# Kernel tuning notes

Measured on AMD Instinct MI355X. Metric: run time of the kernel, lower is better.

Reference implementation:

```python
import jax, jax.numpy as jnp
import numpy as np

KX = jnp.array([[-1., 0., 1.], [-2., 0., 2.], [-1., 0., 1.]], dtype=jnp.float32).reshape(1, 1, 3, 3)
KY = jnp.array([[1., 2., 1.], [0., 0., 0.], [-1., -2., -1.]], dtype=jnp.float32).reshape(1, 1, 3, 3)

def _sobel(x, k):
    # x: [B,1,H,W], k: [1,1,3,3]; stride 1, padding 1 -> same spatial size
    return jax.lax.conv_general_dilated(
        x, k, window_strides=(1, 1), padding=((1, 1), (1, 1)),
        dimension_numbers=('NCHW', 'OIHW', 'NCHW'))

def setup_inputs() -> dict:
    key = jax.random.key(0)
    k1, k2 = jax.random.split(key)
    B, C, H, W = 32, 1, 512, 512
    output = jax.random.normal(k1, (B, C, H, W), dtype=jnp.float32)
    target = jax.random.normal(k2, (B, C, H, W), dtype=jnp.float32)
    return {"output": output, "target": target}

def reference(output, target):
    gx_t = _sobel(target, KX)
    gy_t = _sobel(target, KY)
    gx_o = _sobel(output, KX)
    gy_o = _sobel(output, KY)
    grad_loss = jnp.mean((gx_t - gx_o) ** 2) + jnp.mean((gy_t - gy_o) ** 2)
    return grad_loss
```

## Files before the change

### kernel.cpp

```cpp
#include <hip/hip_runtime.h>


#define BATCH 32
#define HH 512
#define WW 512
#define RW 4
#define TPB 256
#define NBLK 1024
#define SPI (HH / RW)

__global__ __launch_bounds__(TPB) void sobel_partial_kernel(
    const float* __restrict__ out_img,
    const float* __restrict__ tgt_img,
    float* __restrict__ partials)
{
    const int tid  = threadIdx.x;
    const int lane = tid & 63;
    const int wv   = tid >> 6;
    const int b    = (blockIdx.x & 7) * (NBLK / 8) + (blockIdx.x >> 3);
    const int w    = b * (TPB / 64) + wv;
    const int img  = w >> 7;
    const int y0   = (w & (SPI - 1)) * RW;
    const size_t base = (size_t)img * HH * WW;
    const float* ob = out_img + base + (lane << 3);
    const float* tb = tgt_img + base + (lane << 3);

    float acc = 0.f;

#define DECLROW(j) float4 oA##j, oB##j, tA##j, tB##j, dA##j, dB##j,            \
                          hsA##j, hdA##j, hsB##j, hdB##j;

#define LOADR(j) {                                                             \
    const int gc = min(max(y0 - 1 + (j), 0), HH - 1);                          \
    const float* orow_ = ob + (size_t)gc * WW;                                 \
    const float* trow_ = tb + (size_t)gc * WW;                                 \
    oA##j = *(const float4*)orow_;       oB##j = *(const float4*)(orow_ + 4);  \
    tA##j = *(const float4*)trow_;       tB##j = *(const float4*)(trow_ + 4);  }

#define DIFFH(j) {                                                             \
    const float m_ = ((unsigned)(y0 - 1 + (j)) < (unsigned)HH) ? 1.f : 0.f;    \
    dA##j = make_float4(m_*(tA##j.x-oA##j.x), m_*(tA##j.y-oA##j.y),            \
                        m_*(tA##j.z-oA##j.z), m_*(tA##j.w-oA##j.w));           \
    dB##j = make_float4(m_*(tB##j.x-oB##j.x), m_*(tB##j.y-oB##j.y),            \
                        m_*(tB##j.z-oB##j.z), m_*(tB##j.w-oB##j.w));           \
    float dl_ = __shfl_up(dB##j.w, 1, 64);   if (lane == 0)  dl_ = 0.f;        \
    float dr_ = __shfl_down(dA##j.x, 1, 64); if (lane == 63) dr_ = 0.f;        \
    hsA##j.x = fmaf(2.f, dA##j.x, dl_ + dA##j.y);                              \
    hdA##j.x = dA##j.y - dl_;                                                  \
    hsA##j.y = fmaf(2.f, dA##j.y, dA##j.x + dA##j.z);                          \
    hdA##j.y = dA##j.z - dA##j.x;                                              \
    hsA##j.z = fmaf(2.f, dA##j.z, dA##j.y + dA##j.w);                          \
    hdA##j.z = dA##j.w - dA##j.y;                                              \
    hsA##j.w = fmaf(2.f, dA##j.w, dA##j.z + dB##j.x);                          \
    hdA##j.w = dB##j.x - dA##j.z;                                              \
    hsB##j.x = fmaf(2.f, dB##j.x, dA##j.w + dB##j.y);                          \
    hdB##j.x = dB##j.y - dA##j.w;                                              \
    hsB##j.y = fmaf(2.f, dB##j.y, dB##j.x + dB##j.z);                          \
    hdB##j.y = dB##j.z - dB##j.x;                                              \
    hsB##j.z = fmaf(2.f, dB##j.z, dB##j.y + dB##j.w);                          \
    hdB##j.z = dB##j.w - dB##j.y;                                              \
    hsB##j.w = fmaf(2.f, dB##j.w, dB##j.z + dr_);                              \
    hdB##j.w = dr_ - dB##j.z;                                                  }

#define VP1(S, a, bb, c) {                                                     \
    float gx_, gy_;                                                            \
    gx_ = fmaf(2.f, hd##S##bb.x, hd##S##a.x + hd##S##c.x);                     \
    gy_ = hs##S##a.x - hs##S##c.x;                                             \
    acc = fmaf(gx_, gx_, acc); acc = fmaf(gy_, gy_, acc);                      \
    gx_ = fmaf(2.f, hd##S##bb.y, hd##S##a.y + hd##S##c.y);                     \
    gy_ = hs##S##a.y - hs##S##c.y;                                             \
    acc = fmaf(gx_, gx_, acc); acc = fmaf(gy_, gy_, acc);                      \
    gx_ = fmaf(2.f, hd##S##bb.z, hd##S##a.z + hd##S##c.z);                     \
    gy_ = hs##S##a.z - hs##S##c.z;                                             \
    acc = fmaf(gx_, gx_, acc); acc = fmaf(gy_, gy_, acc);                      \
    gx_ = fmaf(2.f, hd##S##bb.w, hd##S##a.w + hd##S##c.w);                     \
    gy_ = hs##S##a.w - hs##S##c.w;                                             \
    acc = fmaf(gx_, gx_, acc); acc = fmaf(gy_, gy_, acc);                      }
#define VPASS(a, bb, c) VP1(A, a, bb, c) VP1(B, a, bb, c)

    DECLROW(0) DECLROW(1) DECLROW(2) DECLROW(3) DECLROW(4) DECLROW(5)

    LOADR(0) LOADR(1) LOADR(2) LOADR(3)
    DIFFH(0) DIFFH(1)
    LOADR(4)
    DIFFH(2) VPASS(0, 1, 2)
    LOADR(5)
    DIFFH(3) VPASS(1, 2, 3)
    DIFFH(4) VPASS(2, 3, 4)
    DIFFH(5) VPASS(3, 4, 5)

#undef DECLROW
#undef LOADR
#undef DIFFH
#undef VP1
#undef VPASS

    #pragma unroll
    for (int off = 32; off > 0; off >>= 1)
        acc += __shfl_down(acc, off, 64);
    __shared__ float wsum[TPB / 64];
    if (lane == 0) wsum[wv] = acc;
    __syncthreads();
    if (tid == 0)
        partials[b] = wsum[0] + wsum[1] + wsum[2] + wsum[3];
}

__global__ __launch_bounds__(TPB) void reduce_partials_kernel(
    const float* __restrict__ partials, float* __restrict__ out)
{
    const int tid = threadIdx.x;
    const float4 v = *(const float4*)(partials + tid * 4);
    float s = (v.x + v.y) + (v.z + v.w);
    #pragma unroll
    for (int off = 32; off > 0; off >>= 1)
        s += __shfl_down(s, off, 64);
    __shared__ float wsum[TPB / 64];
    if ((tid & 63) == 0) wsum[tid >> 6] = s;
    __syncthreads();
    if (tid == 0)
        out[0] = (wsum[0] + wsum[1] + wsum[2] + wsum[3])
               * (1.0f / ((float)BATCH * HH * WW));
}

extern "C" void kernel_launch(void* const* d_in, const int* in_sizes, int n_in,
                              void* d_out, int out_size, void* d_ws, size_t ws_size,
                              hipStream_t stream) {
    (void)in_sizes; (void)n_in; (void)ws_size; (void)out_size;
    const float* out_img = (const float*)d_in[0];
    const float* tgt_img = (const float*)d_in[1];
    float* partials = (float*)d_ws;
    float* res = (float*)d_out;

    sobel_partial_kernel<<<NBLK, TPB, 0, stream>>>(out_img, tgt_img, partials);
    reduce_partials_kernel<<<1, TPB, 0, stream>>>(partials, res);
}
```

Baseline: 18.62 us.

## Process eight rows per wave with rotating register ring and bigger blocks

Result: no change. 18.82 us (median of 2 runs) (+1.1%).

```diff
diff --git a/kernel.cpp b/kernel.cpp
--- a/kernel.cpp
+++ b/kernel.cpp
@@ -4,10 +4,9 @@
 #define BATCH 32
 #define HH 512
 #define WW 512
-#define RW 4
-#define TPB 256
-#define NBLK 1024
-#define SPI (HH / RW)
+#define RW 8
+#define TPB 512
+#define NBLK 256
 
 __global__ __launch_bounds__(TPB) void sobel_partial_kernel(
     const float* __restrict__ out_img,
@@ -18,81 +17,75 @@
     const int lane = tid & 63;
     const int wv   = tid >> 6;
     const int b    = (blockIdx.x & 7) * (NBLK / 8) + (blockIdx.x >> 3);
-    const int w    = b * (TPB / 64) + wv;
-    const int img  = w >> 7;
-    const int y0   = (w & (SPI - 1)) * RW;
+    const int img  = b >> 3;
+    const int y0   = ((b & 7) * 8 + wv) * RW;
     const size_t base = (size_t)img * HH * WW;
     const float* ob = out_img + base + (lane << 3);
     const float* tb = tgt_img + base + (lane << 3);
 
     float acc = 0.f;
 
-#define DECLROW(j) float4 oA##j, oB##j, tA##j, tB##j, dA##j, dB##j,            \
-                          hsA##j, hdA##j, hsB##j, hdB##j;
+#define DECLL(k) float4 oA##k, oB##k, tA##k, tB##k;
+#define DECLH(h) float4 hsA##h, hdA##h, hsB##h, hdB##h;
+    DECLL(0) DECLL(1) DECLL(2) DECLL(3)
+    DECLH(0) DECLH(1) DECLH(2)
 
-#define LOADR(j) {                                                             \
-    const int gc = min(max(y0 - 1 + (j), 0), HH - 1);                          \
-    const float* orow_ = ob + (size_t)gc * WW;                                 \
-    const float* trow_ = tb + (size_t)gc * WW;                                 \
-    oA##j = *(const float4*)orow_;       oB##j = *(const float4*)(orow_ + 4);  \
-    tA##j = *(const float4*)trow_;       tB##j = *(const float4*)(trow_ + 4);  }
+#define LOADR(i, k) {                                                          \
+    const int gc_ = min(max(y0 - 1 + (i), 0), HH - 1);                         \
+    const float* o_ = ob + (size_t)gc_ * WW;                                   \
+    const float* t_ = tb + (size_t)gc_ * WW;                                   \
+    oA##k = *(const float4*)o_;  oB##k = *(const float4*)(o_ + 4);             \
+    tA##k = *(const float4*)t_;  tB##k = *(const float4*)(t_ + 4);             }
 
-#define DIFFH(j) {                                                             \
-    const float m_ = ((unsigned)(y0 - 1 + (j)) < (unsigned)HH) ? 1.f : 0.f;    \
-    dA##j = make_float4(m_*(tA##j.x-oA##j.x), m_*(tA##j.y-oA##j.y),            \
-                        m_*(tA##j.z-oA##j.z), m_*(tA##j.w-oA##j.w));           \
-    dB##j = make_float4(m_*(tB##j.x-oB##j.x), m_*(tB##j.y-oB##j.y),            \
-                        m_*(tB##j.z-oB##j.z), m_*(tB##j.w-oB##j.w));           \
-    float dl_ = __shfl_up(dB##j.w, 1, 64);   if (lane == 0)  dl_ = 0.f;        \
-    float dr_ = __shfl_down(dA##j.x, 1, 64); if (lane == 63) dr_ = 0.f;        \
-    hsA##j.x = fmaf(2.f, dA##j.x, dl_ + dA##j.y);                              \
-    hdA##j.x = dA##j.y - dl_;                                                  \
-    hsA##j.y = fmaf(2.f, dA##j.y, dA##j.x + dA##j.z);                          \
-    hdA##j.y = dA##j.z - dA##j.x;                                              \
-    hsA##j.z = fmaf(2.f, dA##j.z, dA##j.y + dA##j.w);                          \
-    hdA##j.z = dA##j.w - dA##j.y;                                              \
-    hsA##j.w = fmaf(2.f, dA##j.w, dA##j.z + dB##j.x);                          \
-    hdA##j.w = dB##j.x - dA##j.z;                                              \
-    hsB##j.x = fmaf(2.f, dB##j.x, dA##j.w + dB##j.y);                          \
-    hdB##j.x = dB##j.y - dA##j.w;                                              \
-    hsB##j.y = fmaf(2.f, dB##j.y, dB##j.x + dB##j.z);                          \
-    hdB##j.y = dB##j.z - dB##j.x;                                              \
-    hsB##j.z = fmaf(2.f, dB##j.z, dB##j.y + dB##j.w);                          \
-    hdB##j.z = dB##j.w - dB##j.y;                                              \
-    hsB##j.w = fmaf(2.f, dB##j.w, dB##j.z + dr_);                              \
-    hdB##j.w = dr_ - dB##j.z;                                                  }
+#define DIFFH(i, k, h) {                                                       \
+    const float m_ = ((unsigned)(y0 - 1 + (i)) < (unsigned)HH) ? 1.f : 0.f;    \
+    const float4 dA_ = make_float4(m_*(tA##k.x-oA##k.x), m_*(tA##k.y-oA##k.y), \
+                                   m_*(tA##k.z-oA##k.z), m_*(tA##k.w-oA##k.w));\
+    const float4 dB_ = make_float4(m_*(tB##k.x-oB##k.x), m_*(tB##k.y-oB##k.y), \
+                                   m_*(tB##k.z-oB##k.z), m_*(tB##k.w-oB##k.w));\
+    float dl_ = __shfl_up(dB_.w, 1, 64);   if (lane == 0)  dl_ = 0.f;          \
+    float dr_ = __shfl_down(dA_.x, 1, 64); if (lane == 63) dr_ = 0.f;          \
+    hsA##h.x = fmaf(2.f, dA_.x, dl_ + dA_.y);   hdA##h.x = dA_.y - dl_;        \
+    hsA##h.y = fmaf(2.f, dA_.y, dA_.x + dA_.z); hdA##h.y = dA_.z - dA_.x;      \
+    hsA##h.z = fmaf(2.f, dA_.z, dA_.y + dA_.w); hdA##h.z = dA_.w - dA_.y;      \
+    hsA##h.w = fmaf(2.f, dA_.w, dA_.z + dB_.x); hdA##h.w = dB_.x - dA_.z;      \
+    hsB##h.x = fmaf(2.f, dB_.x, dA_.w + dB_.y); hdB##h.x = dB_.y - dA_.w;      \
+    hsB##h.y = fmaf(2.f, dB_.y, dB_.x + dB_.z); hdB##h.y = dB_.z - dB_.x;      \
+    hsB##h.z = fmaf(2.f, dB_.z, dB_.y + dB_.w); hdB##h.z = dB_.w - dB_.y;      \
+    hsB##h.w = fmaf(2.f, dB_.w, dB_.z + dr_);   hdB##h.w = dr_ - dB_.z;        }
 
-#define VP1(S, a, bb, c) {                                                     \
-    float gx_, gy_;                                                            \
-    gx_ = fmaf(2.f, hd##S##bb.x, hd##S##a.x + hd##S##c.x);                     \
-    gy_ = hs##S##a.x - hs##S##c.x;                                             \
-    acc = fmaf(gx_, gx_, acc); acc = fmaf(gy_, gy_, acc);                      \
-    gx_ = fmaf(2.f, hd##S##bb.y, hd##S##a.y + hd##S##c.y);                     \
-    gy_ = hs##S##a.y - hs##S##c.y;                                             \
-    acc = fmaf(gx_, gx_, acc); acc = fmaf(gy_, gy_, acc);                      \
-    gx_ = fmaf(2.f, hd##S##bb.z, hd##S##a.z + hd##S##c.z);                     \
-    gy_ = hs##S##a.z - hs##S##c.z;                                             \
-    acc = fmaf(gx_, gx_, acc); acc = fmaf(gy_, gy_, acc);                      \
-    gx_ = fmaf(2.f, hd##S##bb.w, hd##S##a.w + hd##S##c.w);                     \
-    gy_ = hs##S##a.w - hs##S##c.w;                                             \
+#define VP4(S, T, M, Bt, c) {                                                  \
+    const float gx_ = fmaf(2.f, hd##S##M.c, hd##S##T.c + hd##S##Bt.c);         \
+    const float gy_ = hs##S##T.c - hs##S##Bt.c;                                \
     acc = fmaf(gx_, gx_, acc); acc = fmaf(gy_, gy_, acc);                      }
-#define VPASS(a, bb, c) VP1(A, a, bb, c) VP1(B, a, bb, c)
+#define VPASS(T, M, Bt)                                                        \
+    VP4(A, T, M, Bt, x) VP4(A, T, M, Bt, y) VP4(A, T, M, Bt, z)                \
+    VP4(A, T, M, Bt, w) VP4(B, T, M, Bt, x) VP4(B, T, M, Bt, y)                \
+    VP4(B, T, M, Bt, z) VP4(B, T, M, Bt, w)
 
-    DECLROW(0) DECLROW(1) DECLROW(2) DECLROW(3) DECLROW(4) DECLROW(5)
+    LOADR(0, 0) LOADR(1, 1) LOADR(2, 2) LOADR(3, 3)
+    DIFFH(0, 0, 0)
+    DIFFH(1, 1, 1)
+    LOADR(4, 0)
+    DIFFH(2, 2, 2) VPASS(0, 1, 2)
+    LOADR(5, 1)
+    DIFFH(3, 3, 0) VPASS(1, 2, 0)
+    LOADR(6, 2)
+    DIFFH(4, 0, 1) VPASS(2, 0, 1)
+    LOADR(7, 3)
+    DIFFH(5, 1, 2) VPASS(0, 1, 2)
+    LOADR(8, 0)
+    DIFFH(6, 2, 0) VPASS(1, 2, 0)
+    LOADR(9, 1)
+    DIFFH(7, 3, 1) VPASS(2, 0, 1)
+    DIFFH(8, 0, 2) VPASS(0, 1, 2)
+    DIFFH(9, 1, 0) VPASS(1, 2, 0)
 
-    LOADR(0) LOADR(1) LOADR(2) LOADR(3)
-    DIFFH(0) DIFFH(1)
-    LOADR(4)
-    DIFFH(2) VPASS(0, 1, 2)
-    LOADR(5)
-    DIFFH(3) VPASS(1, 2, 3)
-    DIFFH(4) VPASS(2, 3, 4)
-    DIFFH(5) VPASS(3, 4, 5)
-
-#undef DECLROW
+#undef DECLL
+#undef DECLH
 #undef LOADR
 #undef DIFFH
-#undef VP1
+#undef VP4
 #undef VPASS
 
     #pragma unroll
@@ -101,20 +94,23 @@
     __shared__ float wsum[TPB / 64];
     if (lane == 0) wsum[wv] = acc;
     __syncthreads();
-    if (tid == 0)
-        partials[b] = wsum[0] + wsum[1] + wsum[2] + wsum[3];
+    if (tid == 0) {
+        float s = 0.f;
+        #pragma unroll
+        for (int k = 0; k < TPB / 64; ++k) s += wsum[k];
+        partials[b] = s;
+    }
 }
 
-__global__ __launch_bounds__(TPB) void reduce_partials_kernel(
+__global__ __launch_bounds__(256) void reduce_partials_kernel(
     const float* __restrict__ partials, float* __restrict__ out)
 {
     const int tid = threadIdx.x;
-    const float4 v = *(const float4*)(partials + tid * 4);
-    float s = (v.x + v.y) + (v.z + v.w);
+    float s = partials[tid];
     #pragma unroll
     for (int off = 32; off > 0; off >>= 1)
         s += __shfl_down(s, off, 64);
-    __shared__ float wsum[TPB / 64];
+    __shared__ float wsum[4];
     if ((tid & 63) == 0) wsum[tid >> 6] = s;
     __syncthreads();
     if (tid == 0)
@@ -132,5 +128,5 @@
     float* res = (float*)d_out;
 
     sobel_partial_kernel<<<NBLK, TPB, 0, stream>>>(out_img, tgt_img, partials);
-    reduce_partials_kernel<<<1, TPB, 0, stream>>>(partials, res);
+    reduce_partials_kernel<<<1, 256, 0, stream>>>(partials, res);
 }
```
